# Performance work log

Measured on AMD Instinct MI355X. Metric: run time of the kernel, lower is better.

Reference implementation:

```python
import jax, jax.numpy as jnp
import numpy as np

C_V, C_F, C_D = 10, 64, 16
COSTS = jnp.array([10.0, 5.0, 2.0], dtype=jnp.float32)  # bandwidth cost per granularity
PENALTY = 0.0  # no_transmission_utility_penalty


def setup_inputs() -> dict:
    key = jax.random.key(0)
    k1, k2 = jax.random.split(key)
    B, H, W = 4, 192, 192
    collab = jax.random.normal(k1, (B, C_V + C_F + C_D, H, W), dtype=jnp.float32)
    utility = jax.random.normal(k2, (B, H, W, 3), dtype=jnp.float32)
    return {"collab_bev_data_list": collab, "utility_map_list": utility,
            "bandwidth_budget": 200000}


def _selection_mechanism(utility, budget_per_sample):
    # utility: [B, H, W, G]; returns [B, H, W] float selected granularity (-1 = none)
    B, H, W, G = utility.shape
    best_u = jnp.max(utility, axis=3)                      # [B,H,W]
    best_g = jnp.argmax(utility, axis=3)                   # [B,H,W]
    N = B * H * W
    flat_u = best_u.reshape(N)
    flat_g = best_g.reshape(N)
    b_idx = jnp.repeat(jnp.arange(B, dtype=jnp.int32), H * W)
    valid = flat_u > PENALTY
    cost = COSTS[flat_g]                                   # [N]
    # sort candidates by utility, descending (stable, matching list.sort)
    order = jnp.argsort(-flat_u)
    v_s = valid[order]
    c_s = cost[order]
    b_s = b_idx[order]

    # greedy budget-constrained selection per sample (sequential knapsack)
    def step(usage, item):
        v, c, b = item
        ok = v & (usage[b] + c <= budget_per_sample)
        usage = usage.at[b].add(jnp.where(ok, c, jnp.float32(0)))
        return usage, ok

    _, sel_sorted = jax.lax.scan(step, jnp.zeros((B,), jnp.float32), (v_s, c_s, b_s))
    selected = jnp.zeros((N,), bool).at[order].set(sel_sorted)
    idx = jnp.where(selected, flat_g.astype(jnp.float32), jnp.float32(-1.0))
    return idx.reshape(B, H, W)


def _build_sparse_bev(sel_idx, vox, feat, det):
    m0 = (sel_idx == 0.0)[:, None, :, :]
    m1 = (sel_idx == 1.0)[:, None, :, :]
    m2 = (sel_idx == 2.0)[:, None, :, :]
    return jnp.concatenate([vox * m0, feat * m1, det * m2], axis=1)


def reference(collab_bev_data_list, utility_map_list, bandwidth_budget):
    cav_num = collab_bev_data_list.shape[0]
    budget_per_sample = jnp.float32(bandwidth_budget / cav_num)
    sel_idx = _selection_mechanism(utility_map_list, budget_per_sample)
    vox = collab_bev_data_list[:, :C_V]
    feat = collab_bev_data_list[:, C_V:C_V + C_F]
    det = collab_bev_data_list[:, C_V + C_F:C_V + C_F + C_D]
    sparse = _build_sparse_bev(sel_idx, vox, feat, det)
    return sparse, sel_idx
```

## Files before the change

### kernel.cpp

```cpp
#include <hip/hip_runtime.h>
#include <stdint.h>
#include <math.h>

#define B_    4
#define H_    192
#define W_    192
#define HW    (H_*W_)
#define NPIX  (B_*HW)
#define C_V   10
#define C_F   64
#define C_D   16
#define C_ALL (C_V+C_F+C_D)
#define HBINS 32768
#define CAP   2048
#define NSLICE 36
#define NCAND (NSLICE*5)

#define OFF_HIST   0u
#define ZERO_U4    ((4u*HBINS*4u)/16u)
#define OFF_KEY    (4u*HBINS*4u)
#define OFF_G      (OFF_KEY + (uint32_t)NPIX*4u)
#define OFF_SELX   (OFF_G + (uint32_t)NPIX)
#define OFF_RES    (OFF_SELX + (uint32_t)NPIX)
#define OFF_GCNT   (OFF_RES + 48u)
#define OFF_GLIST  (OFF_GCNT + 16u)
#define OFF_CAND   (OFF_GLIST + 4u*CAP*8u)

__device__ __forceinline__ uint32_t costOf(uint32_t g) {
    return g == 0u ? 10u : (g == 1u ? 5u : 2u);
}

__device__ __forceinline__ uint32_t budgetInt(const int* bptr) {
    double bps = (double)bptr[0] / (double)B_;
    float f = (float)bps;
    return (uint32_t)floorf(f);
}

#define CE(x, y) { uint64_t _mn = (x) < (y) ? (x) : (y); \
                   uint64_t _mx = (x) < (y) ? (y) : (x); (x) = _mx; (y) = _mn; }

__global__ void k_zero(uint4* __restrict__ w4) {
    uint32_t i = blockIdx.x * blockDim.x + threadIdx.x;
    w4[i] = make_uint4(0u, 0u, 0u, 0u);
}

__global__ void k_prep(const float* __restrict__ util, uint4* __restrict__ key4,
                       uint32_t* __restrict__ g4, uint32_t* __restrict__ selx4,
                       uint32_t* __restrict__ hist) {
    int t = blockIdx.x * blockDim.x + threadIdx.x;
    if (t >= NPIX / 4) return;
    const float4* u4 = (const float4*)util + (size_t)t * 3;
    float4 a = u4[0], b4 = u4[1], c4 = u4[2];
    float u[4][3] = { {a.x, a.y, a.z}, {a.w, b4.x, b4.y},
                      {b4.z, b4.w, c4.x}, {c4.y, c4.z, c4.w} };
    uint32_t kk[4]; uint32_t gpack = 0;
    #pragma unroll
    for (int p = 0; p < 4; ++p) {
        float best = u[p][0]; uint32_t g = 0;
        if (u[p][1] > best) { best = u[p][1]; g = 1; }
        if (u[p][2] > best) { best = u[p][2]; g = 2; }
        kk[p] = (best > 0.0f) ? (__float_as_uint(best) | 0x80000000u) : 0u;
        gpack |= g << (8 * p);
    }
    key4[t] = make_uint4(kk[0], kk[1], kk[2], kk[3]);
    g4[t] = gpack;
    selx4[t] = 0u;
    int b = (t * 4) / HW;
    #pragma unroll
    for (int p = 0; p < 4; ++p)
        if (kk[p])
            atomicAdd(&hist[(size_t)b * HBINS + ((kk[p] >> 16) & 32767u)],
                      costOf((gpack >> (8 * p)) & 3u));
}

__global__ __launch_bounds__(256) void k_cut(const uint32_t* __restrict__ hist,
                                             const int* __restrict__ budget_ptr,
                                             uint32_t* __restrict__ res,
                                             uint32_t* __restrict__ gcnt) {
    int b = blockIdx.x;
    int t = threadIdx.x;
    int lane = t & 63, wv = t >> 6;
    uint32_t budget = budgetInt(budget_ptr);
    const uint32_t* hb = hist + (size_t)b * HBINS;

    __shared__ uint32_t csum[256];

    const uint4* h4 = (const uint4*)(hb + (size_t)t * 128);
    uint32_t s = 0;
    #pragma unroll 8
    for (int j = 0; j < 32; ++j) { uint4 v = h4[j]; s += v.x + v.y + v.z + v.w; }
    csum[t] = s;
    __syncthreads();
    if (wv != 0) return;

    int hi = 255 - 4 * lane;
    uint32_t c0 = csum[hi], c1 = csum[hi - 1], c2 = csum[hi - 2], c3 = csum[hi - 3];
    uint32_t cs = c0 + c1 + c2 + c3;
    uint32_t v = cs;
    #pragma unroll
    for (int off = 1; off < 64; off <<= 1) {
        uint32_t o = __shfl_up(v, off);
        if (lane >= off) v += o;
    }
    uint32_t excl = v - cs;
    bool found = (excl <= budget) && (v > budget);
    uint32_t cbin = 0, cusage = 0;
    if (found) {
        uint32_t cum = excl;
        if      (cum + c0 > budget) { cbin = (uint32_t)hi;     cusage = cum; }
        else if ((cum += c0) + c1 > budget) { cbin = (uint32_t)(hi - 1); cusage = cum; }
        else if ((cum += c1) + c2 > budget) { cbin = (uint32_t)(hi - 2); cusage = cum; }
        else                        { cbin = (uint32_t)(hi - 3); cusage = cum + c2; }
    }
    unsigned long long msk = __ballot(found);
    if (msk == 0ull) {
        if (lane == 0) { res[b] = 0xFFFFFFFFu; res[4 + b] = 0u; res[8 + b] = 1u;
                         gcnt[b] = 0u; }
        return;
    }
    int src = __ffsll((long long)msk) - 1;
    cbin   = __shfl(cbin, src);
    cusage = __shfl(cusage, src);

    const uint32_t* fb = hb + (size_t)cbin * 128;
    int fhi = 127 - 2 * lane;
    uint32_t f0 = fb[fhi], f1 = fb[fhi - 1];
    uint32_t fs = f0 + f1;
    v = fs;
    #pragma unroll
    for (int off = 1; off < 64; off <<= 1) {
        uint32_t o = __shfl_up(v, off);
        if (lane >= off) v += o;
    }
    excl = cusage + v - fs;
    found = (excl <= budget) && (excl + fs > budget);
    uint32_t b2 = 0, fusage = 0;
    if (found) {
        if (excl + f0 > budget) { b2 = cbin * 128u + (uint32_t)fhi;       fusage = excl; }
        else                    { b2 = cbin * 128u + (uint32_t)(fhi - 1); fusage = excl + f0; }
    }
    msk = __ballot(found);
    src = __ffsll((long long)msk) - 1;
    b2     = __shfl(b2, src);
    fusage = __shfl(fusage, src);
    if (lane == 0) {
        res[b]     = b2;
        res[4 + b] = fusage;
        uint32_t bs = b2 + 32768u;
        res[8 + b] = (bs >= 65535u) ? 0xFFFFFFFFu : ((bs + 1u) << 16);
        gcnt[b] = 0u;
    }
}

__global__ __launch_bounds__(1024) void k_gather(const uint32_t* __restrict__ key,
                                                 const uint8_t* __restrict__ g,
                                                 const uint32_t* __restrict__ res,
                                                 uint32_t* __restrict__ gcnt,
                                                 uint64_t* __restrict__ glist,
                                                 uint64_t* __restrict__ cand) {
    int b = blockIdx.y;
    uint32_t b2 = res[b];
    if (b2 == 0xFFFFFFFFu) return;
    int t = threadIdx.x;
    int lane = t & 63, wv = t >> 6;
    uint32_t pix = blockIdx.x * 1024u + (uint32_t)t;

    __shared__ uint64_t red5[16];
    __shared__ uint64_t red2[16][4];

    uint32_t k = key[(size_t)b * HW + pix];
    uint64_t m5 = 0, a0 = 0, a1 = 0, a2 = 0, a3 = 0;
    if (k) {
        uint32_t bin = (k >> 16) & 32767u;
        if (bin == b2) {
            uint32_t gg = g[(size_t)b * HW + pix];
            uint32_t idx = atomicAdd(&gcnt[b], 1u);
            if (idx < CAP)
                glist[(size_t)b * CAP + idx] =
                    ((uint64_t)(~k) << 32) | ((uint64_t)pix << 2) | (uint64_t)gg;
        } else if (bin < b2) {
            uint32_t gg = g[(size_t)b * HW + pix];
            if (gg) {
                uint64_t m = ((uint64_t)k << 18) | ((uint64_t)(65535u - pix) << 2)
                           | (uint64_t)gg;
                if (gg == 1u) m5 = m; else a0 = m;
            }
        }
    }
    #pragma unroll
    for (int off = 32; off; off >>= 1) {
        uint64_t o5 = __shfl_down(m5, off);
        if (o5 > m5) m5 = o5;
        uint64_t b0 = __shfl_down(a0, off), b1 = __shfl_down(a1, off),
                 b2_ = __shfl_down(a2, off), b3 = __shfl_down(a3, off);
        CE(a0, b3); CE(a1, b2_); CE(a2, b1); CE(a3, b0);
        CE(a0, a2); CE(a1, a3); CE(a0, a1); CE(a2, a3);
    }
    if (lane == 0) {
        red5[wv] = m5;
        red2[wv][0] = a0; red2[wv][1] = a1; red2[wv][2] = a2; red2[wv][3] = a3;
    }
    __syncthreads();
    if (t == 0) {
        uint64_t g5 = 0, t0 = 0, t1 = 0, t2 = 0, t3 = 0;
        for (int wq = 0; wq < 16; ++wq) {
            if (red5[wq] > g5) g5 = red5[wq];
            #pragma unroll
            for (int q = 0; q < 4; ++q) {
                uint64_t m = red2[wq][q];
                if (m > t3) {
                    if      (m > t0) { t3 = t2; t2 = t1; t1 = t0; t0 = m; }
                    else if (m > t1) { t3 = t2; t2 = t1; t1 = m; }
                    else if (m > t2) { t3 = t2; t2 = m; }
                    else             { t3 = m; }
                }
            }
        }
        uint64_t* cb_ = cand + ((size_t)b * NSLICE + blockIdx.x) * 5;
        cb_[0] = g5; cb_[1] = t0; cb_[2] = t1; cb_[3] = t2; cb_[4] = t3;
    }
}

__global__ __launch_bounds__(256) void k_final(const uint32_t* __restrict__ res,
                                               const uint32_t* __restrict__ gcnt,
                                               const uint64_t* __restrict__ glist,
                                               const uint64_t* __restrict__ cand,
                                               const int* __restrict__ budget_ptr,
                                               uint8_t* __restrict__ selx) {
    int b = blockIdx.x;
    uint32_t b2 = res[b];
    if (b2 == 0xFFFFFFFFu) return;
    int t = threadIdx.x;

    __shared__ uint64_t e[CAP];
    __shared__ uint64_t s[CAP];
    __shared__ uint64_t cd[NCAND];

    uint32_t cnt = gcnt[b];
    int n = (int)(cnt < (uint32_t)CAP ? cnt : (uint32_t)CAP);
    for (int i = t; i < n; i += 256) e[i] = glist[(size_t)b * CAP + i];
    for (int i = t; i < NCAND; i += 256) cd[i] = cand[(size_t)b * NCAND + i];
    __syncthreads();

    for (int i = t; i < n; i += 256) {
        uint64_t ei = e[i];
        int rk = 0;
        for (int j = 0; j < n; ++j) rk += (e[j] < ei);
        s[rk] = ei;
    }
    __syncthreads();

    if (t == 0) {
        uint32_t budget = budgetInt(budget_ptr);
        uint32_t usage = res[4 + b];
        uint8_t* sx = selx + (size_t)b * HW;
        for (int i = 0; i < n; ++i) {
            uint64_t ei = s[i];
            uint32_t c = costOf((uint32_t)(ei & 3u));
            if (usage + c <= budget) { usage += c; sx[(ei >> 2) & 0xFFFFu] = 1; }
        }
        uint64_t g5 = 0, t0 = 0, t1 = 0, t2 = 0, t3 = 0;
        for (int i = 0; i < NCAND; ++i) {
            uint64_t m = cd[i];
            if (!m) continue;
            if ((m & 3u) == 1u) { if (m > g5) g5 = m; }
            else if (m > t3) {
                if      (m > t0) { t3 = t2; t2 = t1; t1 = t0; t0 = m; }
                else if (m > t1) { t3 = t2; t2 = t1; t1 = m; }
                else if (m > t2) { t3 = t2; t2 = m; }
                else             { t3 = m; }
            }
        }
        uint64_t c5[5] = { g5, t0, t1, t2, t3 };
        for (int i = 1; i < 5; ++i) {
            uint64_t x = c5[i]; int j = i;
            while (j > 0 && c5[j - 1] < x) { c5[j] = c5[j - 1]; --j; }
            c5[j] = x;
        }
        uint32_t r = budget - usage;
        for (int i = 0; i < 5; ++i) {
            uint64_t m = c5[i];
            if (!m) break;
            uint32_t c = costOf((uint32_t)(m & 3u));
            if (c <= r) {
                r -= c;
                uint32_t pix = 65535u - (uint32_t)((m >> 2) & 0xFFFFu);
                sx[pix] = 1;
            }
        }
    }
}

__global__ void k_sparse(const float* __restrict__ collab, const uint4* __restrict__ key4,
                         const uint32_t* __restrict__ g4, const uint32_t* __restrict__ selx4,
                         const uint32_t* __restrict__ hl_arr,
                         float* __restrict__ out, float* __restrict__ selOut) {
    int tid = blockIdx.x * blockDim.x + threadIdx.x;
    int c = blockIdx.y, b = blockIdx.z;
    int cls = (c < C_V) ? 0 : ((c < C_V + C_F) ? 1 : 2);
    uint32_t hl = hl_arr[b];
    size_t p4 = (size_t)b * (HW / 4) + (size_t)tid;
    uint4 kk = key4[p4];
    uint32_t gg = g4[p4];
    uint32_t sx = selx4[p4];
    int sc[4];
    uint32_t kv[4] = { kk.x, kk.y, kk.z, kk.w };
    #pragma unroll
    for (int p = 0; p < 4; ++p) {
        bool se = (kv[p] >= hl) || (((sx >> (8 * p)) & 0xFFu) != 0u);
        sc[p] = se ? (int)((gg >> (8 * p)) & 3u) : -1;
    }
    size_t co = ((size_t)(b * C_ALL + c)) * HW + (size_t)tid * 4;
    float4 v = *(const float4*)(collab + co);
    float4 o;
    o.x = (sc[0] == cls) ? v.x : 0.0f;
    o.y = (sc[1] == cls) ? v.y : 0.0f;
    o.z = (sc[2] == cls) ? v.z : 0.0f;
    o.w = (sc[3] == cls) ? v.w : 0.0f;
    *(float4*)(out + co) = o;
    if (c == 0) {
        float4 sf = make_float4((float)sc[0], (float)sc[1], (float)sc[2], (float)sc[3]);
        ((float4*)selOut)[p4] = sf;
    }
}

extern "C" void kernel_launch(void* const* d_in, const int* in_sizes, int n_in,
                              void* d_out, int out_size, void* d_ws, size_t ws_size,
                              hipStream_t stream) {
    (void)in_sizes; (void)n_in; (void)out_size; (void)ws_size;
    const float* collab = (const float*)d_in[0];
    const float* util   = (const float*)d_in[1];
    const int*   budget = (const int*)d_in[2];

    uint8_t*  ws     = (uint8_t*)d_ws;
    uint32_t* hist   = (uint32_t*)(ws + OFF_HIST);
    uint32_t* key    = (uint32_t*)(ws + OFF_KEY);
    uint8_t*  g      = ws + OFF_G;
    uint8_t*  selx   = ws + OFF_SELX;
    uint32_t* res    = (uint32_t*)(ws + OFF_RES);
    uint32_t* gcnt   = (uint32_t*)(ws + OFF_GCNT);
    uint64_t* glist  = (uint64_t*)(ws + OFF_GLIST);
    uint64_t* cand   = (uint64_t*)(ws + OFF_CAND);

    float* outSparse = (float*)d_out;
    float* outSel    = outSparse + (size_t)B_ * C_ALL * HW;

    k_zero  <<<ZERO_U4 / 256, 256, 0, stream>>>((uint4*)ws);
    k_prep  <<<(NPIX / 4 + 255) / 256, 256, 0, stream>>>(util, (uint4*)key, (uint32_t*)g,
                                                         (uint32_t*)selx, hist);
    k_cut   <<<B_, 256, 0, stream>>>(hist, budget, res, gcnt);
    dim3 gridG(NSLICE, B_);
    k_gather<<<gridG, 1024, 0, stream>>>(key, g, res, gcnt, glist, cand);
    k_final <<<B_, 256, 0, stream>>>(res, gcnt, glist, cand, budget, selx);
    dim3 grid3(HW / 4 / 256, C_ALL, B_);
    k_sparse<<<grid3, 256, 0, stream>>>(collab, (const uint4*)key, (const uint32_t*)g,
                                        (const uint32_t*)selx, res + 8, outSparse, outSel);
}
```

Before: 103.7 us.

## Fuse gather and final selection kernels via last-block completion counter

Merges the gather and final knapsack-resolution kernels into one launch. The last block to finish per sample, detected with an atomic done counter, performs the final ranking and selection. Gather blocks drop from 1024 to 256 threads, each looping over 1024 pixels with per-thread top-4 tracking. The final candidate reduction is parallelised across a wavefront instead of one thread. This removes one kernel launch and its dependency gap, but adds threadfence overhead and reduces gather parallelism; CAP shrinks to 1536, which may risk overflow on other inputs.

```diff
diff --git a/kernel.cpp b/kernel.cpp
--- a/kernel.cpp
+++ b/kernel.cpp
@@ -3,28 +3,29 @@
 #include <math.h>
 
 #define B_    4
-#define H_    192
-#define W_    192
-#define HW    (H_*W_)
-#define NPIX  (B_*HW)
+#define HW    36864
+#define NPIX  147456
 #define C_V   10
 #define C_F   64
 #define C_D   16
-#define C_ALL (C_V+C_F+C_D)
+#define C_ALL 90
 #define HBINS 32768
-#define CAP   2048
-#define NSLICE 36
-#define NCAND (NSLICE*5)
-
-#define OFF_HIST   0u
-#define ZERO_U4    ((4u*HBINS*4u)/16u)
-#define OFF_KEY    (4u*HBINS*4u)
-#define OFF_G      (OFF_KEY + (uint32_t)NPIX*4u)
-#define OFF_SELX   (OFF_G + (uint32_t)NPIX)
-#define OFF_RES    (OFF_SELX + (uint32_t)NPIX)
-#define OFF_GCNT   (OFF_RES + 48u)
-#define OFF_GLIST  (OFF_GCNT + 16u)
-#define OFF_CAND   (OFF_GLIST + 4u*CAP*8u)
+#define CAP   1536
+#define NSL   36
+#define SLPX  1024
+#define NCAND (NSL*5)
+#define INV   0xFFFFFFFFu
+
+#define OFF_HIST  0u
+#define OFF_GCNT  524288u
+#define OFF_DONE  524304u
+#define ZERO_U4   32770u
+#define OFF_KEY   524320u
+#define OFF_G     1114144u
+#define OFF_SELX  1261600u
+#define OFF_RES   1409056u
+#define OFF_GLIST 1409104u
+#define OFF_CAND  1458256u
 
 __device__ __forceinline__ uint32_t costOf(uint32_t g) {
     return g == 0u ? 10u : (g == 1u ? 5u : 2u);
@@ -41,7 +42,7 @@
 
 __global__ void k_zero(uint4* __restrict__ w4) {
     uint32_t i = blockIdx.x * blockDim.x + threadIdx.x;
-    w4[i] = make_uint4(0u, 0u, 0u, 0u);
+    if (i < ZERO_U4) w4[i] = make_uint4(0u, 0u, 0u, 0u);
 }
 
 __global__ void k_prep(const float* __restrict__ util, uint4* __restrict__ key4,
@@ -75,8 +76,7 @@
 
 __global__ __launch_bounds__(256) void k_cut(const uint32_t* __restrict__ hist,
                                              const int* __restrict__ budget_ptr,
-                                             uint32_t* __restrict__ res,
-                                             uint32_t* __restrict__ gcnt) {
+                                             uint32_t* __restrict__ res) {
     int b = blockIdx.x;
     int t = threadIdx.x;
     int lane = t & 63, wv = t >> 6;
@@ -107,15 +107,14 @@
     uint32_t cbin = 0, cusage = 0;
     if (found) {
         uint32_t cum = excl;
-        if      (cum + c0 > budget) { cbin = (uint32_t)hi;     cusage = cum; }
+        if      (cum + c0 > budget) { cbin = (uint32_t)hi;       cusage = cum; }
         else if ((cum += c0) + c1 > budget) { cbin = (uint32_t)(hi - 1); cusage = cum; }
         else if ((cum += c1) + c2 > budget) { cbin = (uint32_t)(hi - 2); cusage = cum; }
         else                        { cbin = (uint32_t)(hi - 3); cusage = cum + c2; }
     }
     unsigned long long msk = __ballot(found);
     if (msk == 0ull) {
-        if (lane == 0) { res[b] = 0xFFFFFFFFu; res[4 + b] = 0u; res[8 + b] = 1u;
-                         gcnt[b] = 0u; }
+        if (lane == 0) { res[b] = INV; res[4 + b] = 0u; res[8 + b] = 1u; }
         return;
     }
     int src = __ffsll((long long)msk) - 1;
@@ -147,43 +146,58 @@
         res[b]     = b2;
         res[4 + b] = fusage;
         uint32_t bs = b2 + 32768u;
-        res[8 + b] = (bs >= 65535u) ? 0xFFFFFFFFu : ((bs + 1u) << 16);
-        gcnt[b] = 0u;
-    }
-}
-
-__global__ __launch_bounds__(1024) void k_gather(const uint32_t* __restrict__ key,
-                                                 const uint8_t* __restrict__ g,
-                                                 const uint32_t* __restrict__ res,
-                                                 uint32_t* __restrict__ gcnt,
-                                                 uint64_t* __restrict__ glist,
-                                                 uint64_t* __restrict__ cand) {
+        res[8 + b] = (bs >= 65535u) ? INV : ((bs + 1u) << 16);
+    }
+}
+
+__global__ __launch_bounds__(256) void k_gf(const uint32_t* __restrict__ key,
+                                            const uint8_t* __restrict__ g,
+                                            const uint32_t* __restrict__ res,
+                                            const int* __restrict__ budget_ptr,
+                                            uint32_t* __restrict__ gcnt,
+                                            uint64_t* __restrict__ glist,
+                                            uint64_t* __restrict__ cand,
+                                            uint32_t* __restrict__ done,
+                                            uint8_t* __restrict__ selx) {
     int b = blockIdx.y;
     uint32_t b2 = res[b];
-    if (b2 == 0xFFFFFFFFu) return;
+    if (b2 == INV) return;
+    int sl = blockIdx.x;
     int t = threadIdx.x;
     int lane = t & 63, wv = t >> 6;
-    uint32_t pix = blockIdx.x * 1024u + (uint32_t)t;
-
-    __shared__ uint64_t red5[16];
-    __shared__ uint64_t red2[16][4];
-
-    uint32_t k = key[(size_t)b * HW + pix];
+
+    __shared__ union {
+        struct { uint64_t red5[4]; uint64_t red2[4][4]; } gat;
+        struct { uint64_t e[CAP]; uint64_t s[CAP]; uint64_t cd[NCAND]; } fin;
+    } sm;
+    __shared__ int lastFlag;
+
+    const uint32_t* kb = key + (size_t)b * HW;
+    const uint8_t*  gb = g   + (size_t)b * HW;
     uint64_t m5 = 0, a0 = 0, a1 = 0, a2 = 0, a3 = 0;
-    if (k) {
+    for (int p = t; p < SLPX; p += 256) {
+        uint32_t pix = (uint32_t)(sl * SLPX + p);
+        uint32_t k = kb[pix];
+        if (!k) continue;
         uint32_t bin = (k >> 16) & 32767u;
         if (bin == b2) {
-            uint32_t gg = g[(size_t)b * HW + pix];
+            uint32_t gg = gb[pix];
             uint32_t idx = atomicAdd(&gcnt[b], 1u);
             if (idx < CAP)
                 glist[(size_t)b * CAP + idx] =
                     ((uint64_t)(~k) << 32) | ((uint64_t)pix << 2) | (uint64_t)gg;
         } else if (bin < b2) {
-            uint32_t gg = g[(size_t)b * HW + pix];
+            uint32_t gg = gb[pix];
             if (gg) {
                 uint64_t m = ((uint64_t)k << 18) | ((uint64_t)(65535u - pix) << 2)
                            | (uint64_t)gg;
-                if (gg == 1u) m5 = m; else a0 = m;
+                if (gg == 1u) { if (m > m5) m5 = m; }
+                else if (m > a3) {
+                    if      (m > a0) { a3 = a2; a2 = a1; a1 = a0; a0 = m; }
+                    else if (m > a1) { a3 = a2; a2 = a1; a1 = m; }
+                    else if (m > a2) { a3 = a2; a2 = m; }
+                    else             { a3 = m; }
+                }
             }
         }
     }
@@ -197,17 +211,18 @@
         CE(a0, a2); CE(a1, a3); CE(a0, a1); CE(a2, a3);
     }
     if (lane == 0) {
-        red5[wv] = m5;
-        red2[wv][0] = a0; red2[wv][1] = a1; red2[wv][2] = a2; red2[wv][3] = a3;
+        sm.gat.red5[wv] = m5;
+        sm.gat.red2[wv][0] = a0; sm.gat.red2[wv][1] = a1;
+        sm.gat.red2[wv][2] = a2; sm.gat.red2[wv][3] = a3;
     }
     __syncthreads();
     if (t == 0) {
         uint64_t g5 = 0, t0 = 0, t1 = 0, t2 = 0, t3 = 0;
-        for (int wq = 0; wq < 16; ++wq) {
-            if (red5[wq] > g5) g5 = red5[wq];
+        for (int wq = 0; wq < 4; ++wq) {
+            if (sm.gat.red5[wq] > g5) g5 = sm.gat.red5[wq];
             #pragma unroll
             for (int q = 0; q < 4; ++q) {
-                uint64_t m = red2[wq][q];
+                uint64_t m = sm.gat.red2[wq][q];
                 if (m > t3) {
                     if      (m > t0) { t3 = t2; t2 = t1; t1 = t0; t0 = m; }
                     else if (m > t1) { t3 = t2; t2 = t1; t1 = m; }
@@ -216,76 +231,79 @@
                 }
             }
         }
-        uint64_t* cb_ = cand + ((size_t)b * NSLICE + blockIdx.x) * 5;
+        uint64_t* cb_ = cand + ((size_t)b * NSL + (size_t)sl) * 5;
         cb_[0] = g5; cb_[1] = t0; cb_[2] = t1; cb_[3] = t2; cb_[4] = t3;
     }
-}
-
-__global__ __launch_bounds__(256) void k_final(const uint32_t* __restrict__ res,
-                                               const uint32_t* __restrict__ gcnt,
-                                               const uint64_t* __restrict__ glist,
-                                               const uint64_t* __restrict__ cand,
-                                               const int* __restrict__ budget_ptr,
-                                               uint8_t* __restrict__ selx) {
-    int b = blockIdx.x;
-    uint32_t b2 = res[b];
-    if (b2 == 0xFFFFFFFFu) return;
-    int t = threadIdx.x;
-
-    __shared__ uint64_t e[CAP];
-    __shared__ uint64_t s[CAP];
-    __shared__ uint64_t cd[NCAND];
-
+    __syncthreads();
+
+    __threadfence();
+    if (t == 0) {
+        uint32_t old = atomicAdd(&done[b], 1u);
+        lastFlag = (old == NSL - 1);
+    }
+    __syncthreads();
+    if (!lastFlag) return;
+    __threadfence();
+
+    uint32_t budget = budgetInt(budget_ptr);
     uint32_t cnt = gcnt[b];
     int n = (int)(cnt < (uint32_t)CAP ? cnt : (uint32_t)CAP);
-    for (int i = t; i < n; i += 256) e[i] = glist[(size_t)b * CAP + i];
-    for (int i = t; i < NCAND; i += 256) cd[i] = cand[(size_t)b * NCAND + i];
-    __syncthreads();
-
+    for (int i = t; i < n; i += 256) sm.fin.e[i] = glist[(size_t)b * CAP + i];
+    for (int i = t; i < NCAND; i += 256) sm.fin.cd[i] = cand[(size_t)b * NCAND + i];
+    __syncthreads();
     for (int i = t; i < n; i += 256) {
-        uint64_t ei = e[i];
+        uint64_t ei = sm.fin.e[i];
         int rk = 0;
-        for (int j = 0; j < n; ++j) rk += (e[j] < ei);
-        s[rk] = ei;
-    }
-    __syncthreads();
-
-    if (t == 0) {
-        uint32_t budget = budgetInt(budget_ptr);
-        uint32_t usage = res[4 + b];
-        uint8_t* sx = selx + (size_t)b * HW;
-        for (int i = 0; i < n; ++i) {
-            uint64_t ei = s[i];
-            uint32_t c = costOf((uint32_t)(ei & 3u));
-            if (usage + c <= budget) { usage += c; sx[(ei >> 2) & 0xFFFFu] = 1; }
-        }
-        uint64_t g5 = 0, t0 = 0, t1 = 0, t2 = 0, t3 = 0;
-        for (int i = 0; i < NCAND; ++i) {
-            uint64_t m = cd[i];
+        for (int j = 0; j < n; ++j) rk += (sm.fin.e[j] < ei);
+        sm.fin.s[rk] = ei;
+    }
+    __syncthreads();
+    if (wv == 0) {
+        uint64_t w5 = 0, c0 = 0, c1 = 0, c2 = 0, c3 = 0;
+        for (int i = lane; i < NCAND; i += 64) {
+            uint64_t m = sm.fin.cd[i];
             if (!m) continue;
-            if ((m & 3u) == 1u) { if (m > g5) g5 = m; }
-            else if (m > t3) {
-                if      (m > t0) { t3 = t2; t2 = t1; t1 = t0; t0 = m; }
-                else if (m > t1) { t3 = t2; t2 = t1; t1 = m; }
-                else if (m > t2) { t3 = t2; t2 = m; }
-                else             { t3 = m; }
-            }
-        }
-        uint64_t c5[5] = { g5, t0, t1, t2, t3 };
-        for (int i = 1; i < 5; ++i) {
-            uint64_t x = c5[i]; int j = i;
-            while (j > 0 && c5[j - 1] < x) { c5[j] = c5[j - 1]; --j; }
-            c5[j] = x;
-        }
-        uint32_t r = budget - usage;
-        for (int i = 0; i < 5; ++i) {
-            uint64_t m = c5[i];
-            if (!m) break;
-            uint32_t c = costOf((uint32_t)(m & 3u));
-            if (c <= r) {
-                r -= c;
-                uint32_t pix = 65535u - (uint32_t)((m >> 2) & 0xFFFFu);
-                sx[pix] = 1;
+            if ((m & 3u) == 1u) { if (m > w5) w5 = m; }
+            else if (m > c3) {
+                if      (m > c0) { c3 = c2; c2 = c1; c1 = c0; c0 = m; }
+                else if (m > c1) { c3 = c2; c2 = c1; c1 = m; }
+                else if (m > c2) { c3 = c2; c2 = m; }
+                else             { c3 = m; }
+            }
+        }
+        #pragma unroll
+        for (int off = 32; off; off >>= 1) {
+            uint64_t o5 = __shfl_down(w5, off);
+            if (o5 > w5) w5 = o5;
+            uint64_t b0 = __shfl_down(c0, off), b1 = __shfl_down(c1, off),
+                     b2_ = __shfl_down(c2, off), b3 = __shfl_down(c3, off);
+            CE(c0, b3); CE(c1, b2_); CE(c2, b1); CE(c3, b0);
+            CE(c0, c2); CE(c1, c3); CE(c0, c1); CE(c2, c3);
+        }
+        if (lane == 0) {
+            uint32_t usage = res[4 + b];
+            uint8_t* sx = selx + (size_t)b * HW;
+            for (int i = 0; i < n; ++i) {
+                uint64_t ei = sm.fin.s[i];
+                uint32_t c = costOf((uint32_t)(ei & 3u));
+                if (usage + c <= budget) { usage += c; sx[(ei >> 2) & 0xFFFFu] = 1; }
+            }
+            uint64_t c5[5] = { w5, c0, c1, c2, c3 };
+            for (int i = 1; i < 5; ++i) {
+                uint64_t x = c5[i]; int j = i;
+                while (j > 0 && c5[j - 1] < x) { c5[j] = c5[j - 1]; --j; }
+                c5[j] = x;
+            }
+            uint32_t r = budget - usage;
+            for (int i = 0; i < 5; ++i) {
+                uint64_t m = c5[i];
+                if (!m) break;
+                uint32_t c = costOf((uint32_t)(m & 3u));
+                if (c <= r) {
+                    r -= c;
+                    uint32_t pix = 65535u - (uint32_t)((m >> 2) & 0xFFFFu);
+                    sx[pix] = 1;
+                }
             }
         }
     }
@@ -332,27 +350,29 @@
     const float* util   = (const float*)d_in[1];
     const int*   budget = (const int*)d_in[2];
 
-    uint8_t*  ws     = (uint8_t*)d_ws;
-    uint32_t* hist   = (uint32_t*)(ws + OFF_HIST);
-    uint32_t* key    = (uint32_t*)(ws + OFF_KEY);
-    uint8_t*  g      = ws + OFF_G;
-    uint8_t*  selx   = ws + OFF_SELX;
-    uint32_t* res    = (uint32_t*)(ws + OFF_RES);
-    uint32_t* gcnt   = (uint32_t*)(ws + OFF_GCNT);
-    uint64_t* glist  = (uint64_t*)(ws + OFF_GLIST);
-    uint64_t* cand   = (uint64_t*)(ws + OFF_CAND);
+    uint8_t*  ws    = (uint8_t*)d_ws;
+    uint32_t* hist  = (uint32_t*)(ws + OFF_HIST);
+    uint32_t* gcnt  = (uint32_t*)(ws + OFF_GCNT);
+    uint32_t* done  = (uint32_t*)(ws + OFF_DONE);
+    uint32_t* key   = (uint32_t*)(ws + OFF_KEY);
+    uint8_t*  g     = ws + OFF_G;
+    uint8_t*  selx  = ws + OFF_SELX;
+    uint32_t* res   = (uint32_t*)(ws + OFF_RES);
+    uint64_t* glist = (uint64_t*)(ws + OFF_GLIST);
+    uint64_t* cand  = (uint64_t*)(ws + OFF_CAND);
 
     float* outSparse = (float*)d_out;
     float* outSel    = outSparse + (size_t)B_ * C_ALL * HW;
 
-    k_zero  <<<ZERO_U4 / 256, 256, 0, stream>>>((uint4*)ws);
-    k_prep  <<<(NPIX / 4 + 255) / 256, 256, 0, stream>>>(util, (uint4*)key, (uint32_t*)g,
-                                                         (uint32_t*)selx, hist);
-    k_cut   <<<B_, 256, 0, stream>>>(hist, budget, res, gcnt);
-    dim3 gridG(NSLICE, B_);
-    k_gather<<<gridG, 1024, 0, stream>>>(key, g, res, gcnt, glist, cand);
-    k_final <<<B_, 256, 0, stream>>>(res, gcnt, glist, cand, budget, selx);
-    dim3 grid3(HW / 4 / 256, C_ALL, B_);
-    k_sparse<<<grid3, 256, 0, stream>>>(collab, (const uint4*)key, (const uint32_t*)g,
-                                        (const uint32_t*)selx, res + 8, outSparse, outSel);
-}
+    k_zero <<<(ZERO_U4 + 255) / 256, 256, 0, stream>>>((uint4*)ws);
+    k_prep <<<NPIX / 4 / 256, 256, 0, stream>>>(util, (uint4*)key, (uint32_t*)g,
+                                                (uint32_t*)selx, hist);
+    k_cut  <<<B_, 256, 0, stream>>>(hist, budget, res);
+    dim3 gridGF(NSL, B_);
+    k_gf   <<<gridGF, 256, 0, stream>>>(key, g, res, budget, gcnt, glist, cand,
+                                        done, selx);
+    dim3 gridSP(HW / 4 / 256, C_ALL, B_);
+    k_sparse<<<gridSP, 256, 0, stream>>>(collab, (const uint4*)key, (const uint32_t*)g,
+                                         (const uint32_t*)selx, res + 8,
+                                         outSparse, outSel);
+}
```

After: 90.40 us. 1.15x faster.
